# Kernel tuning notes

Hardware: AMD Instinct MI355X
Metric: run time of the kernel (lower is better)

## Reference

```python
import jax, jax.numpy as jnp
import numpy as np

C = 256
C4 = C // 4  # 64
B = 4
N = 4096
FACTOR = float(np.sqrt(C4))


def setup_inputs() -> dict:
    key = jax.random.key(0)
    k1, k2, k3, k4 = jax.random.split(key, 4)
    x = jax.random.normal(k1, (B, C, N), dtype=jnp.float32)
    # q_conv and k_conv share the SAME weight (tied in the torch module)
    W_qk = jax.random.normal(k2, (C4, C), dtype=jnp.float32) * (1.0 / np.sqrt(C))
    W_v = jax.random.normal(k3, (C4, C), dtype=jnp.float32) * (1.0 / np.sqrt(C))
    b_v = jax.random.normal(k4, (C4,), dtype=jnp.float32) * 0.01
    return {"x": x, "W_qk": W_qk, "W_v": W_v, "b_v": b_v}


def reference(x, W_qk, W_v, b_v):
    # Conv1d with kernel size 1 == per-position linear: [B,C,N] -> [B,C4,N]
    x_q = jnp.einsum('oc,bcn->bon', W_qk, x)          # [B, C4, N]
    x_k = x_q                                          # tied weights: k == q
    x_v = jnp.einsum('oc,bcn->bon', W_v, x) + b_v[None, :, None]  # [B, C4, N]
    # energy = x_k.permute(0,2,1) @ x_q : [B, N, N]
    energy = jnp.einsum('bcn,bcm->bnm', x_k, x_q) / FACTOR
    attention = jax.nn.softmax(energy, axis=-1)        # softmax over last dim
    x_r = jnp.einsum('bcn,bnm->bcm', x_v, attention)   # [B, C4, N]
    return x_r
```

## Files before the change

kernel.cpp:

```cpp
#include <hip/hip_runtime.h>


#define CC 256
#define C4C 64
#define NBATCH 4
#define NN 4096
#define QSCALE 0.42466089f
#define SHIFT2 12.0f

typedef _Float16 f16;
typedef _Float16 half2v __attribute__((ext_vector_type(2)));
typedef _Float16 half4 __attribute__((ext_vector_type(4)));
typedef _Float16 half8 __attribute__((ext_vector_type(8)));
typedef __fp16 fp16x2 __attribute__((ext_vector_type(2)));
typedef float floatx4 __attribute__((ext_vector_type(4)));

static __device__ __forceinline__ half2v pkrtz(float a, float b) {
  fp16x2 r = __builtin_amdgcn_cvt_pkrtz(a, b);
  return __builtin_bit_cast(half2v, r);
}

#define LOADQ(T, A0, A1)                                                   \
  { const f16* p_ = Qb + (size_t)(T) * 1024 + l * 8;                       \
    A0 = *(const half8*)(p_); A1 = *(const half8*)(p_ + 512); }

#define XT_PITCH 264
__global__ __launch_bounds__(256) void qv_kernel(
    const float* __restrict__ x, const float* __restrict__ Wqk,
    const float* __restrict__ Wv, const float* __restrict__ bv,
    f16* __restrict__ Qtb, f16* __restrict__ V4)
{
  __shared__ __align__(16) f16 xt[32][XT_PITCH];
  const int b = blockIdx.y;
  const int n0 = blockIdx.x * 32;
  const int tid = threadIdx.x;

  {
    const int nq = tid & 7;
    const int cb = tid >> 3;
    const int c = cb * 8;
    const float* xp = x + (size_t)b * CC * NN + n0 + nq * 4;
    float4 r[8];
#pragma unroll
    for (int j = 0; j < 8; ++j)
      r[j] = *(const float4*)(xp + (size_t)(c + j) * NN);
#pragma unroll
    for (int s = 0; s < 4; ++s) {
      half8 h;
#pragma unroll
      for (int j = 0; j < 8; ++j) h[j] = (f16)(((const float*)&r[j])[s]);
      *(half8*)(&xt[nq * 4 + s][c]) = h;
    }
  }

  const int w = tid >> 6, l = tid & 63, lr = l & 15, lg = l >> 4;
  const float* Wsrc = (w < 2) ? Wqk : Wv;
  const int ocb = (w & 1) * 32;
  half8 af[2][8];
#pragma unroll
  for (int t = 0; t < 2; ++t) {
    const float* wp = Wsrc + (size_t)(ocb + t * 16 + lr) * CC + 8 * lg;
#pragma unroll
    for (int kk = 0; kk < 8; ++kk) {
      float4 wa = *(const float4*)(wp + kk * 32);
      float4 wb = *(const float4*)(wp + kk * 32 + 4);
      half8 h;
      h[0] = (f16)wa.x; h[1] = (f16)wa.y; h[2] = (f16)wa.z; h[3] = (f16)wa.w;
      h[4] = (f16)wb.x; h[5] = (f16)wb.y; h[6] = (f16)wb.z; h[7] = (f16)wb.w;
      af[t][kk] = h;
    }
  }

  __syncthreads();

  floatx4 acc[2][2] = {{{0.f,0.f,0.f,0.f},{0.f,0.f,0.f,0.f}},
                       {{0.f,0.f,0.f,0.f},{0.f,0.f,0.f,0.f}}};
#pragma unroll
  for (int nt = 0; nt < 2; ++nt) {
#pragma unroll
    for (int kk = 0; kk < 8; ++kk) {
      half8 bf = *(const half8*)(&xt[nt * 16 + lr][kk * 32 + 8 * lg]);
      acc[0][nt] = __builtin_amdgcn_mfma_f32_16x16x32_f16(af[0][kk], bf, acc[0][nt], 0, 0, 0);
      acc[1][nt] = __builtin_amdgcn_mfma_f32_16x16x32_f16(af[1][kk], bf, acc[1][nt], 0, 0, 0);
    }
  }

  if (w < 2) {
#pragma unroll
    for (int t = 0; t < 2; ++t)
#pragma unroll
      for (int nt = 0; nt < 2; ++nt) {
        int T = (n0 >> 4) + nt;
        int kg = 2 * t + (lg >> 1);
        union { f16 h[4]; unsigned long long u; } q4;
#pragma unroll
        for (int i = 0; i < 4; ++i) q4.h[i] = (f16)(acc[t][nt][i] * QSCALE);
        *(unsigned long long*)(Qtb + (size_t)(b * 256 + T) * 1024 + w * 512
                               + (kg * 16 + lr) * 8 + (lg & 1) * 4) = q4.u;
      }
  } else {
#pragma unroll
    for (int t = 0; t < 2; ++t)
#pragma unroll
      for (int nt = 0; nt < 2; ++nt) {
        int T = (n0 >> 4) + nt;
        int oc = (w - 2) * 32 + t * 16 + 4 * lg;
#pragma unroll
        for (int i = 0; i < 4; ++i)
          V4[(size_t)(b * 256 + T) * 1024 + (oc + i) * 16 + lr] =
              (f16)(acc[t][nt][i] + bv[oc + i]);
      }
  }
}

#define Z_PRELOAD(TBEG)                                                    \
  { _Pragma("unroll")                                                      \
    for (int mt = 0; mt < 8; ++mt) {                                       \
      const f16* p_ = Qb + (size_t)((TBEG) + mt) * 1024 + l * 8;           \
      bb[mt][0] = *(const half8*)(p_);                                     \
      bb[mt][1] = *(const half8*)(p_ + 512);                               \
    } }

#define Z_E(MT, D0, D1)                                                    \
  { D0 = (floatx4){0.f,0.f,0.f,0.f}; D1 = (floatx4){0.f,0.f,0.f,0.f};      \
    D0 = __builtin_amdgcn_mfma_f32_16x16x32_f16(a[0][0], bb[MT][0], D0, 0, 0, 0); \
    D1 = __builtin_amdgcn_mfma_f32_16x16x32_f16(a[1][0], bb[MT][0], D1, 0, 0, 0); \
    D0 = __builtin_amdgcn_mfma_f32_16x16x32_f16(a[0][1], bb[MT][1], D0, 0, 0, 0); \
    D1 = __builtin_amdgcn_mfma_f32_16x16x32_f16(a[1][1], bb[MT][1], D1, 0, 0, 0); }

#define Z_SM(D0, D1)                                                       \
  { _Pragma("unroll")                                                      \
    for (int i = 0; i < 4; ++i) {                                          \
      rs[0][i] += __builtin_amdgcn_exp2f(D0[i]);                           \
      rs[1][i] += __builtin_amdgcn_exp2f(D1[i]); } }

#define Z_TILES17                                                          \
  Z_E(1, dB0, dB1); Z_SM(dA0, dA1);                                        \
  Z_E(2, dA0, dA1); Z_SM(dB0, dB1);                                        \
  Z_E(3, dB0, dB1); Z_SM(dA0, dA1);                                        \
  Z_E(4, dA0, dA1); Z_SM(dB0, dB1);                                        \
  Z_E(5, dB0, dB1); Z_SM(dA0, dA1);                                        \
  Z_E(6, dA0, dA1); Z_SM(dB0, dB1);                                        \
  Z_E(7, dB0, dB1); Z_SM(dA0, dA1);

__global__ __launch_bounds__(256) void z_kernel(
    const f16* __restrict__ Qtb, float* __restrict__ Zp)
{
  __shared__ float zl[4][32];
  const int bx = blockIdx.x;
  const int xcd = bx & 7, slot = bx >> 3;
  const int b = xcd >> 1;
  const int wu = ((xcd & 1) << 7) | slot;
  const int n0 = (wu >> 1) * 32;
  const int mh = wu & 1;
  const int tid = threadIdx.x;
  const int w = tid >> 6, l = tid & 63, lr = l & 15, lg = l >> 4;
  const f16* Qb = Qtb + (size_t)b * 256 * 1024;

  half8 a[2][2];
  LOADQ((n0 >> 4), a[0][0], a[0][1]);
  LOADQ((n0 >> 4) + 1, a[1][0], a[1][1]);

  const int tstr = mh * 128 + w * 32;
  half8 bb[8][2];
  floatx4 dA0, dA1, dB0, dB1;
  float rs[2][4] = {{0.f,0.f,0.f,0.f},{0.f,0.f,0.f,0.f}};

  Z_PRELOAD(tstr);
  Z_E(0, dA0, dA1);
  Z_TILES17;
#pragma unroll 1
  for (int mch = 1; mch < 4; ++mch) {
    Z_PRELOAD(tstr + mch * 8);
    Z_SM(dB0, dB1);
    Z_E(0, dA0, dA1);
    Z_TILES17;
  }
  Z_SM(dB0, dB1);

#pragma unroll
  for (int t = 0; t < 2; ++t)
#pragma unroll
    for (int i = 0; i < 4; ++i) {
      float v = rs[t][i];
      v += __shfl_xor(v, 1); v += __shfl_xor(v, 2);
      v += __shfl_xor(v, 4); v += __shfl_xor(v, 8);
      rs[t][i] = v;
    }
  if (lr == 0) {
#pragma unroll
    for (int t = 0; t < 2; ++t)
#pragma unroll
      for (int i = 0; i < 4; ++i)
        zl[w][16 * t + 4 * lg + i] = rs[t][i];
  }
  __syncthreads();
  if (tid < 32) {
    float s = zl[0][tid] + zl[1][tid] + zl[2][tid] + zl[3][tid];
    Zp[(size_t)mh * NBATCH * NN + b * NN + n0 + tid] = s;
  }
}

__global__ __launch_bounds__(256) void zr_kernel(
    const float* __restrict__ Zp, float* __restrict__ Zinv)
{
  int i = blockIdx.x * 256 + threadIdx.x;
  Zinv[i] = 4096.0f / (Zp[i] + Zp[(size_t)NBATCH * NN + i]);
}

#define LOADV(NB, UA)                                                      \
  { const f16* up_ = Vb + (size_t)(NB) * 1024 + 4 * lg;                    \
    _Pragma("unroll")                                                      \
    for (int cs = 0; cs < 4; ++cs)                                         \
      UA[cs] = *(const half4*)(up_ + (16 * cs + lr) * 16); }

__global__ __launch_bounds__(512, 4) void av_kernel(
    const f16* __restrict__ Qtb, const f16* __restrict__ V4,
    const float* __restrict__ Zinv, float* __restrict__ Out)
{
  __shared__ float red[8][2][16][17];

  const int bx = blockIdx.x;
  const int xcd = bx & 7, slot = bx >> 3;
  const int b = xcd >> 1;
  const int m0 = (((xcd & 1) << 6) | slot) * 32;
  const int tid = threadIdx.x;
  const int w = tid >> 6;
  const int l = tid & 63;
  const int lr = l & 15, lg = l >> 4;

  const f16* Qb = Qtb + (size_t)b * 256 * 1024;
  const f16* Vb = V4 + (size_t)b * 256 * 1024;
  const float* Zb = Zinv + b * NN;

  half8 bq[2][2];
  LOADQ((m0 >> 4), bq[0][0], bq[0][1]);
  LOADQ((m0 >> 4) + 1, bq[1][0], bq[1][1]);

  floatx4 o[4][2];
#pragma unroll
  for (int cs = 0; cs < 4; ++cs)
#pragma unroll
    for (int t = 0; t < 2; ++t) o[cs][t] = (floatx4){0.f, 0.f, 0.f, 0.f};

#pragma unroll 2
  for (int it = 0; it < 32; ++it) {
    const int T = it * 8 + w;
    half8 a0, a1;
    LOADQ(T, a0, a1);
    half4 va[4];
    LOADV(T, va);
    const float4 zi = *(const float4*)(Zb + T * 16 + 4 * lg);

    floatx4 dA = {-SHIFT2, -SHIFT2, -SHIFT2, -SHIFT2};
    floatx4 dB = {-SHIFT2, -SHIFT2, -SHIFT2, -SHIFT2};
    dA = __builtin_amdgcn_mfma_f32_16x16x32_f16(a0, bq[0][0], dA, 0, 0, 0);
    dB = __builtin_amdgcn_mfma_f32_16x16x32_f16(a0, bq[1][0], dB, 0, 0, 0);
    dA = __builtin_amdgcn_mfma_f32_16x16x32_f16(a1, bq[0][1], dA, 0, 0, 0);
    dB = __builtin_amdgcn_mfma_f32_16x16x32_f16(a1, bq[1][1], dB, 0, 0, 0);

    half2v p0a = pkrtz(__builtin_amdgcn_exp2f(dA[0]) * zi.x,
                       __builtin_amdgcn_exp2f(dA[1]) * zi.y);
    half2v p0b = pkrtz(__builtin_amdgcn_exp2f(dA[2]) * zi.z,
                       __builtin_amdgcn_exp2f(dA[3]) * zi.w);
    half2v p1a = pkrtz(__builtin_amdgcn_exp2f(dB[0]) * zi.x,
                       __builtin_amdgcn_exp2f(dB[1]) * zi.y);
    half2v p1b = pkrtz(__builtin_amdgcn_exp2f(dB[2]) * zi.z,
                       __builtin_amdgcn_exp2f(dB[3]) * zi.w);
    half4 bt0 = {p0a[0], p0a[1], p0b[0], p0b[1]};
    half4 bt1 = {p1a[0], p1a[1], p1b[0], p1b[1]};
#pragma unroll
    for (int cs = 0; cs < 4; ++cs) {
      o[cs][0] = __builtin_amdgcn_mfma_f32_16x16x16f16(va[cs], bt0, o[cs][0], 0, 0, 0);
      o[cs][1] = __builtin_amdgcn_mfma_f32_16x16x16f16(va[cs], bt1, o[cs][1], 0, 0, 0);
    }
  }

#pragma unroll 1
  for (int cs = 0; cs < 4; ++cs) {
    __syncthreads();
#pragma unroll
    for (int t = 0; t < 2; ++t)
#pragma unroll
      for (int i = 0; i < 4; ++i)
        red[w][t][4 * lg + i][lr] = o[cs][t][i];
    __syncthreads();
    const int t = tid >> 8;
    const int r = (tid >> 4) & 15;
    const int col = tid & 15;
    float ssum = 0.f;
#pragma unroll
    for (int ww = 0; ww < 8; ++ww) ssum += red[ww][t][r][col];
    Out[((size_t)b * C4C + cs * 16 + r) * NN + m0 + t * 16 + col] = ssum;
  }
}

extern "C" void kernel_launch(void* const* d_in, const int* in_sizes, int n_in,
                              void* d_out, int out_size, void* d_ws, size_t ws_size,
                              hipStream_t stream)
{
  const float* x   = (const float*)d_in[0];
  const float* Wqk = (const float*)d_in[1];
  const float* Wv  = (const float*)d_in[2];
  const float* bv  = (const float*)d_in[3];
  float* out = (float*)d_out;

  char* ws = (char*)d_ws;
  f16*   Qtb  = (f16*)(ws);
  f16*   V4   = (f16*)(ws + (2u << 20));
  float* Zp   = (float*)(ws + (4u << 20));
  float* Zinv = (float*)(ws + (4u << 20) + (128u << 10));

  qv_kernel<<<dim3(128, 4), 256, 0, stream>>>(x, Wqk, Wv, bv, Qtb, V4);
  z_kernel<<<dim3(1024), 256, 0, stream>>>(Qtb, Zp);
  zr_kernel<<<dim3(64), 256, 0, stream>>>(Zp, Zinv);
  av_kernel<<<dim3(512), 512, 0, stream>>>(Qtb, V4, Zinv, out);
}
```

Measured before the change: 63.03 us.

## Exploit symmetric energy matrix to halve softmax-normalizer computation

Because q and k share weights, the energy matrix is symmetric, so the new z kernel computes only the upper half of the 16x16 tile pairs, using diagonal offsets, and gets both row and column partial sums from each tile. Column sums are stored as fp16 partials in the output buffer, which serves as scratch, and a finalize kernel reduces 8 row partials plus 128 column partials per position. This halves the MFMA and exp work for the normalizer, but adds scattered partial writes and a heavier reduction kernel. The fp16 partial sums also cost some accuracy, and the exp2 values now use a -SHIFT2 offset, so normalization relies on that shift matching the one used in av_kernel.

```diff
diff --git a/kernel.cpp b/kernel.cpp
--- a/kernel.cpp
+++ b/kernel.cpp
@@ -113,99 +113,81 @@
   }
 }
 
-#define Z_PRELOAD(TBEG)                                                    \
-  { _Pragma("unroll")                                                      \
-    for (int mt = 0; mt < 8; ++mt) {                                       \
-      const f16* p_ = Qb + (size_t)((TBEG) + mt) * 1024 + l * 8;           \
-      bb[mt][0] = *(const half8*)(p_);                                     \
-      bb[mt][1] = *(const half8*)(p_ + 512);                               \
-    } }
-
-#define Z_E(MT, D0, D1)                                                    \
-  { D0 = (floatx4){0.f,0.f,0.f,0.f}; D1 = (floatx4){0.f,0.f,0.f,0.f};      \
-    D0 = __builtin_amdgcn_mfma_f32_16x16x32_f16(a[0][0], bb[MT][0], D0, 0, 0, 0); \
-    D1 = __builtin_amdgcn_mfma_f32_16x16x32_f16(a[1][0], bb[MT][0], D1, 0, 0, 0); \
-    D0 = __builtin_amdgcn_mfma_f32_16x16x32_f16(a[0][1], bb[MT][1], D0, 0, 0, 0); \
-    D1 = __builtin_amdgcn_mfma_f32_16x16x32_f16(a[1][1], bb[MT][1], D1, 0, 0, 0); }
-
-#define Z_SM(D0, D1)                                                       \
-  { _Pragma("unroll")                                                      \
-    for (int i = 0; i < 4; ++i) {                                          \
-      rs[0][i] += __builtin_amdgcn_exp2f(D0[i]);                           \
-      rs[1][i] += __builtin_amdgcn_exp2f(D1[i]); } }
-
-#define Z_TILES17                                                          \
-  Z_E(1, dB0, dB1); Z_SM(dA0, dA1);                                        \
-  Z_E(2, dA0, dA1); Z_SM(dB0, dB1);                                        \
-  Z_E(3, dB0, dB1); Z_SM(dA0, dA1);                                        \
-  Z_E(4, dA0, dA1); Z_SM(dB0, dB1);                                        \
-  Z_E(5, dB0, dB1); Z_SM(dA0, dA1);                                        \
-  Z_E(6, dA0, dA1); Z_SM(dB0, dB1);                                        \
-  Z_E(7, dB0, dB1); Z_SM(dA0, dA1);
-
-__global__ __launch_bounds__(256) void z_kernel(
-    const f16* __restrict__ Qtb, float* __restrict__ Zp)
-{
-  __shared__ float zl[4][32];
+__global__ __launch_bounds__(256) void z2_kernel(
+    const f16* __restrict__ Qtb, float* __restrict__ rowp,
+    f16* __restrict__ Zcp)
+{
   const int bx = blockIdx.x;
   const int xcd = bx & 7, slot = bx >> 3;
   const int b = xcd >> 1;
-  const int wu = ((xcd & 1) << 7) | slot;
-  const int n0 = (wu >> 1) * 32;
-  const int mh = wu & 1;
+  const int wu = ((xcd & 1) << 8) | slot;
   const int tid = threadIdx.x;
   const int w = tid >> 6, l = tid & 63, lr = l & 15, lg = l >> 4;
+  const int unit = wu * 4 + w;
+  const int Tn = unit >> 3;
+  const int j = unit & 7;
   const f16* Qb = Qtb + (size_t)b * 256 * 1024;
 
-  half8 a[2][2];
-  LOADQ((n0 >> 4), a[0][0], a[0][1]);
-  LOADQ((n0 >> 4) + 1, a[1][0], a[1][1]);
-
-  const int tstr = mh * 128 + w * 32;
-  half8 bb[8][2];
-  floatx4 dA0, dA1, dB0, dB1;
-  float rs[2][4] = {{0.f,0.f,0.f,0.f},{0.f,0.f,0.f,0.f}};
-
-  Z_PRELOAD(tstr);
-  Z_E(0, dA0, dA1);
-  Z_TILES17;
-#pragma unroll 1
-  for (int mch = 1; mch < 4; ++mch) {
-    Z_PRELOAD(tstr + mch * 8);
-    Z_SM(dB0, dB1);
-    Z_E(0, dA0, dA1);
-    Z_TILES17;
-  }
-  Z_SM(dB0, dB1);
-
-#pragma unroll
-  for (int t = 0; t < 2; ++t)
-#pragma unroll
-    for (int i = 0; i < 4; ++i) {
-      float v = rs[t][i];
-      v += __shfl_xor(v, 1); v += __shfl_xor(v, 2);
-      v += __shfl_xor(v, 4); v += __shfl_xor(v, 8);
-      rs[t][i] = v;
-    }
+  half8 a0, a1;
+  LOADQ(Tn, a0, a1);
+  float rs[4] = {0.f, 0.f, 0.f, 0.f};
+
+  if (j == 0) {
+    floatx4 d = {-SHIFT2, -SHIFT2, -SHIFT2, -SHIFT2};
+    d = __builtin_amdgcn_mfma_f32_16x16x32_f16(a0, a0, d, 0, 0, 0);
+    d = __builtin_amdgcn_mfma_f32_16x16x32_f16(a1, a1, d, 0, 0, 0);
+#pragma unroll
+    for (int i = 0; i < 4; ++i) rs[i] += __builtin_amdgcn_exp2f(d[i]);
+  }
+
+#pragma unroll 2
+  for (int dd = 1; dd <= 16; ++dd) {
+    const int dgl = j * 16 + dd;
+    if (dgl == 128 && Tn >= 128) continue;
+    const int Tm = (Tn + dgl) & 255;
+    half8 b0, b1;
+    LOADQ(Tm, b0, b1);
+    floatx4 d = {-SHIFT2, -SHIFT2, -SHIFT2, -SHIFT2};
+    d = __builtin_amdgcn_mfma_f32_16x16x32_f16(a0, b0, d, 0, 0, 0);
+    d = __builtin_amdgcn_mfma_f32_16x16x32_f16(a1, b1, d, 0, 0, 0);
+    float e0 = __builtin_amdgcn_exp2f(d[0]);
+    float e1 = __builtin_amdgcn_exp2f(d[1]);
+    float e2 = __builtin_amdgcn_exp2f(d[2]);
+    float e3 = __builtin_amdgcn_exp2f(d[3]);
+    rs[0] += e0; rs[1] += e1; rs[2] += e2; rs[3] += e3;
+    float cs = (e0 + e1) + (e2 + e3);
+    cs += __shfl_xor(cs, 16);
+    cs += __shfl_xor(cs, 32);
+    if (lg == 0)
+      Zcp[(size_t)(dgl - 1) * (NBATCH * NN) + b * NN + Tm * 16 + lr] = (f16)cs;
+  }
+
+#pragma unroll
+  for (int i = 0; i < 4; ++i) {
+    float v = rs[i];
+    v += __shfl_xor(v, 1); v += __shfl_xor(v, 2);
+    v += __shfl_xor(v, 4); v += __shfl_xor(v, 8);
+    rs[i] = v;
+  }
   if (lr == 0) {
 #pragma unroll
-    for (int t = 0; t < 2; ++t)
-#pragma unroll
-      for (int i = 0; i < 4; ++i)
-        zl[w][16 * t + 4 * lg + i] = rs[t][i];
-  }
-  __syncthreads();
-  if (tid < 32) {
-    float s = zl[0][tid] + zl[1][tid] + zl[2][tid] + zl[3][tid];
-    Zp[(size_t)mh * NBATCH * NN + b * NN + n0 + tid] = s;
-  }
-}
-
-__global__ __launch_bounds__(256) void zr_kernel(
-    const float* __restrict__ Zp, float* __restrict__ Zinv)
+    for (int i = 0; i < 4; ++i)
+      rowp[(size_t)j * (NBATCH * NN) + b * NN + Tn * 16 + 4 * lg + i] = rs[i];
+  }
+}
+
+__global__ __launch_bounds__(256) void zf_kernel(
+    const float* __restrict__ rowp, const f16* __restrict__ Zcp,
+    float* __restrict__ Zinv)
 {
   int i = blockIdx.x * 256 + threadIdx.x;
-  Zinv[i] = 4096.0f / (Zp[i] + Zp[(size_t)NBATCH * NN + i]);
+  float s = 0.f;
+#pragma unroll
+  for (int k = 0; k < 8; ++k) s += rowp[(size_t)k * (NBATCH * NN) + i];
+#pragma unroll 4
+  for (int ds = 0; ds < 127; ++ds) s += (float)Zcp[(size_t)ds * (NBATCH * NN) + i];
+  if ((i & (NN - 1)) >= 2048) s += (float)Zcp[(size_t)127 * (NBATCH * NN) + i];
+  Zinv[i] = 1.0f / s;
 }
 
 #define LOADV(NB, UA)                                                      \
@@ -308,11 +290,12 @@
   char* ws = (char*)d_ws;
   f16*   Qtb  = (f16*)(ws);
   f16*   V4   = (f16*)(ws + (2u << 20));
-  float* Zp   = (float*)(ws + (4u << 20));
-  float* Zinv = (float*)(ws + (4u << 20) + (128u << 10));
+  float* rowp = (float*)(ws + (4u << 20));
+  float* Zinv = (float*)(ws + (4u << 20) + (512u << 10));
+  f16*   Zcp  = (f16*)d_out;
 
   qv_kernel<<<dim3(128, 4), 256, 0, stream>>>(x, Wqk, Wv, bv, Qtb, V4);
-  z_kernel<<<dim3(1024), 256, 0, stream>>>(Qtb, Zp);
-  zr_kernel<<<dim3(64), 256, 0, stream>>>(Zp, Zinv);
+  z2_kernel<<<dim3(2048), 256, 0, stream>>>(Qtb, rowp, Zcp);
+  zf_kernel<<<dim3(64), 256, 0, stream>>>(rowp, Zcp, Zinv);
   av_kernel<<<dim3(512), 512, 0, stream>>>(Qtb, V4, Zinv, out);
 }
```

After: 79.65 us. +26.4%, slower.
